# Kernel tuning notes

Hardware: AMD Instinct MI355X
Metric: run time of the kernel (lower is better)

## Reference

```python
import jax, jax.numpy as jnp
import numpy as np

NUM_HEADS = 16


def setup_inputs() -> dict:
    key = jax.random.key(0)
    k1, k2, k3 = jax.random.split(key, 3)
    S, B, E = 2048, 4, 1024
    std = float(np.sqrt(2.0 / (E + E)))
    query = jax.random.normal(k1, (S, B, E), dtype=jnp.float32)
    in_proj_weight = jax.random.normal(k2, (3 * E, E), dtype=jnp.float32) * std
    in_proj_bias = jnp.zeros((3 * E,), dtype=jnp.float32)
    out_proj_weight = jax.random.normal(k3, (E, E), dtype=jnp.float32) * std
    out_proj_bias = jnp.zeros((E,), dtype=jnp.float32)
    return {
        "query": query,
        "in_proj_weight": in_proj_weight,
        "in_proj_bias": in_proj_bias,
        "out_proj_weight": out_proj_weight,
        "out_proj_bias": out_proj_bias,
    }


def reference(query, in_proj_weight, in_proj_bias, out_proj_weight, out_proj_bias):
    S, B, E = query.shape
    H = NUM_HEADS
    hd = E // H
    scale = hd ** -0.5
    # fused QKV projection: [S, B, 3E]
    lin = jnp.einsum("sbe,fe->sbf", query, in_proj_weight) + in_proj_bias
    # torch layout: view(S, B*H, 3, hd) -> interleaved [h, {q,k,v}, hd]
    lin = lin.reshape(S, B * H, 3, hd)
    q = lin[:, :, 0, :]  # [S, B*H, hd]
    k = lin[:, :, 1, :]
    v = lin[:, :, 2, :]
    # scores: [B*H, S_q, S_k]
    scores = jnp.einsum("sbd,tbd->bst", q, k) * scale
    attn = jax.nn.softmax(scores.astype(jnp.float32), axis=-1).astype(scores.dtype)
    # context: [S, B*H, hd] -> [S, B, E]
    ctx = jnp.einsum("bst,tbd->sbd", attn, v).reshape(S, B, E)
    out = jnp.einsum("sbe,fe->sbf", ctx, out_proj_weight) + out_proj_bias
    return out
```

## Files before the change

### kernel.cpp

```cpp
#include <hip/hip_runtime.h>
#include <hip/hip_bf16.h>

typedef __hip_bfloat16 bf16;
typedef __attribute__((ext_vector_type(8))) short short8;
typedef __attribute__((ext_vector_type(4))) float floatx4;

#define GLD_LDS(g, l) __builtin_amdgcn_global_load_lds( \
    (const __attribute__((address_space(1))) void*)(g), \
    (__attribute__((address_space(3))) void*)(l), 16, 0, 0)

#define CS 0.18033688f

__global__ __launch_bounds__(256)
void cvt3_kernel(const float* __restrict__ q,  bf16* __restrict__ qo,
                 const float* __restrict__ w1, bf16* __restrict__ w1o,
                 const float* __restrict__ w2, bf16* __restrict__ w2o)
{
    const int i = blockIdx.x * 256 + threadIdx.x;
    const float* src; bf16* dst; long off;
    if (i < 1048576)       { src = q;  dst = qo;  off = (long)i * 8; }
    else if (i < 1441792)  { src = w1; dst = w1o; off = (long)(i - 1048576) * 8; }
    else                   { src = w2; dst = w2o; off = (long)(i - 1441792) * 8; }
    floatx4 a = *(const floatx4*)(src + off);
    floatx4 b = *(const floatx4*)(src + off + 4);
    short8 h;
    #pragma unroll
    for (int e = 0; e < 4; ++e) {
        union { bf16 v; short s; } u0, u1;
        u0.v = __float2bfloat16(a[e]); h[e]     = u0.s;
        u1.v = __float2bfloat16(b[e]); h[e + 4] = u1.s;
    }
    *(short8*)(dst + off) = h;
}

__device__ __forceinline__ void stage_f32(const float* __restrict__ src, int ld,
                                          bf16* lds, int t)
{
    const int sr = t >> 1;
    const int sc = (t & 1) * 16;
    const float* g = src + (long)sr * ld + sc;
    floatx4 f[4];
    #pragma unroll
    for (int i = 0; i < 4; ++i) f[i] = *(const floatx4*)(g + i * 4);
    short8 h[2];
    #pragma unroll
    for (int v = 0; v < 2; ++v)
        #pragma unroll
        for (int e = 0; e < 8; ++e) {
            union { bf16 b; short s; } u;
            u.b = __float2bfloat16(f[v * 2 + (e >> 2)][e & 3]);
            h[v][e] = u.s;
        }
    *(short8*)(lds + sr * 32 + sc)     = h[0];
    *(short8*)(lds + sr * 32 + sc + 8) = h[1];
}

template<int EPI, int AF32, int BF32>
__global__ __launch_bounds__(256, 2)
void gemm_bt(const void* __restrict__ Ap, const void* __restrict__ Bp,
             const float* __restrict__ bias,
             void* __restrict__ o0, bf16* __restrict__ o1, bf16* __restrict__ o2,
             int K, int N)
{
    __shared__ __align__(16) bf16 lA[128 * 32];
    __shared__ __align__(16) bf16 lB[128 * 32];

    const int t    = threadIdx.x;
    const int lane = t & 63;
    const int w    = t >> 6;
    const int mBase = blockIdx.y * 128;
    const int nBase = blockIdx.x * 128;
    const int wr = (w >> 1) * 64;
    const int wc = (w & 1) * 64;

    const int rowL = t >> 2;
    const int colL = (t & 3) * 8;
    const bf16* gA0 = (const bf16*)Ap + (long)(mBase + rowL) * K + colL;
    const bf16* gA1 = (const bf16*)Ap + (long)(mBase + rowL + 64) * K + colL;
    const bf16* gB0 = (const bf16*)Bp + (long)(nBase + rowL) * K + colL;
    const bf16* gB1 = (const bf16*)Bp + (long)(nBase + rowL + 64) * K + colL;
    char* lAb = (char*)lA + w * 1024;
    char* lBb = (char*)lB + w * 1024;

    floatx4 acc[4][4] = {};

    for (int k0 = 0; k0 < K; k0 += 32) {
        if constexpr (AF32) {
            stage_f32((const float*)Ap + (long)mBase * K + k0, K, lA, t);
        } else {
            GLD_LDS(gA0 + k0, lAb);
            GLD_LDS(gA1 + k0, lAb + 4096);
        }
        if constexpr (BF32) {
            stage_f32((const float*)Bp + (long)nBase * K + k0, K, lB, t);
        } else {
            GLD_LDS(gB0 + k0, lBb);
            GLD_LDS(gB1 + k0, lBb + 4096);
        }
        asm volatile("s_waitcnt vmcnt(0)" ::: "memory");
        __syncthreads();

        short8 af[4], bfr[4];
        #pragma unroll
        for (int m = 0; m < 4; ++m)
            af[m] = *(const short8*)(lA + (wr + m * 16 + (lane & 15)) * 32 + (lane >> 4) * 8);
        #pragma unroll
        for (int n = 0; n < 4; ++n)
            bfr[n] = *(const short8*)(lB + (wc + n * 16 + (lane & 15)) * 32 + (lane >> 4) * 8);
        #pragma unroll
        for (int m = 0; m < 4; ++m)
            #pragma unroll
            for (int n = 0; n < 4; ++n)
                acc[m][n] = __builtin_amdgcn_mfma_f32_16x16x32_bf16(af[m], bfr[n], acc[m][n], 0, 0, 0);
        __syncthreads();
    }

    #pragma unroll
    for (int m = 0; m < 4; ++m) {
        #pragma unroll
        for (int n = 0; n < 4; ++n) {
            const int col = nBase + wc + n * 16 + (lane & 15);
            const int r0  = mBase + wr + m * 16 + ((lane >> 4) << 2);
            const float bv = bias[col];
            if constexpr (EPI == 0) {
                const int h   = col / 192;
                const int rem = col % 192;
                const int qkv = rem >> 6;
                const int d   = rem & 63;
                #pragma unroll
                for (int j = 0; j < 4; ++j) {
                    const int r = r0 + j;
                    const int s = r >> 2;
                    const int b = r & 3;
                    const float v = acc[m][n][j] + bv;
                    if (qkv == 0)
                        ((bf16*)o0)[(((((b << 4) + h) << 11) + s) << 6) + d] =
                            __float2bfloat16(v * CS);
                    else if (qkv == 1)
                        o1[(((((b << 4) + h) << 11) + s) << 6) + d] = __float2bfloat16(v);
                    else
                        o2[((((b << 4) + h) << 17)) + (d << 11) + s] = __float2bfloat16(v);
                }
            } else {
                #pragma unroll
                for (int j = 0; j < 4; ++j)
                    ((float*)o0)[(long)(r0 + j) * N + col] = acc[m][n][j] + bv;
            }
        }
    }
}

__global__ __launch_bounds__(256, 2)
void attn_kernel(const bf16* __restrict__ Q, const bf16* __restrict__ Kg,
                 const bf16* __restrict__ Vt, bf16* __restrict__ Ctx)
{
    __shared__ __align__(16) bf16 lK[2][64 * 64];
    __shared__ __align__(16) bf16 lV[2][64 * 64];

    const int t    = threadIdx.x;
    const int lane = t & 63;
    const int w    = t >> 6;
    const int f    = lane & 15;
    const int g    = lane >> 4;
    const int bh   = blockIdx.y;
    const int q0   = blockIdx.x * 128 + w * 32;
    const long hb  = (long)bh * 2048 * 64;
    const bf16* Qh = Q  + hb;
    const bf16* Kh = Kg + hb;
    const bf16* Vh = Vt + hb;

    const int srow = t >> 3;
    const int scol = (t & 7) * 8;
    const int sig0 = (srow & 3) | ((srow & 16) >> 2) | ((srow & 12) << 1);
    const int wb0 = ((srow)      * 128 + scol * 2) ^ (((srow)      & 7) << 4);
    const int wb1 = ((srow + 32) * 128 + scol * 2) ^ (((srow + 32) & 7) << 4);

    short8 qf[2][2];
    #pragma unroll
    for (int m = 0; m < 2; ++m)
        #pragma unroll
        for (int kk = 0; kk < 2; ++kk)
            qf[m][kk] = *(const short8*)(Qh + (q0 + m * 16 + f) * 64 + kk * 32 + g * 8);

    short8 ones;
    #pragma unroll
    for (int e = 0; e < 8; ++e) ones[e] = (short)0x3F80;

    floatx4 o[2][4] = {};
    floatx4 dn[2] = {};

    short8 kR0 = *(const short8*)(Kh + (long)sig0 * 64 + scol);
    short8 kR1 = *(const short8*)(Kh + (long)(sig0 + 32) * 64 + scol);
    short8 vR0 = *(const short8*)(Vh + (long)srow * 2048 + scol);
    short8 vR1 = *(const short8*)(Vh + (long)(srow + 32) * 2048 + scol);
    *(short8*)((char*)lK[0] + wb0) = kR0;
    *(short8*)((char*)lK[0] + wb1) = kR1;
    *(short8*)((char*)lV[0] + wb0) = vR0;
    *(short8*)((char*)lV[0] + wb1) = vR1;
    kR0 = *(const short8*)(Kh + (long)(64 + sig0) * 64 + scol);
    kR1 = *(const short8*)(Kh + (long)(64 + sig0 + 32) * 64 + scol);
    vR0 = *(const short8*)(Vh + (long)srow * 2048 + 64 + scol);
    vR1 = *(const short8*)(Vh + (long)(srow + 32) * 2048 + 64 + scol);
    __syncthreads();

    auto tile = [&](const bf16* curK, const bf16* curV,
                    bf16* nxtK, bf16* nxtV, int t0) __attribute__((always_inline)) {
        short8 kf[4][2];
        #pragma unroll
        for (int n = 0; n < 4; ++n)
            #pragma unroll
            for (int kk = 0; kk < 2; ++kk) {
                const int key = n * 16 + f;
                const int byte = (key * 128 + kk * 64 + g * 16) ^ ((key & 7) << 4);
                kf[n][kk] = *(const short8*)((const char*)curK + byte);
            }

        if (t0 + 64 < 2048) {
            *(short8*)((char*)nxtK + wb0) = kR0;
            *(short8*)((char*)nxtK + wb1) = kR1;
            *(short8*)((char*)nxtV + wb0) = vR0;
            *(short8*)((char*)nxtV + wb1) = vR1;
        }
        if (t0 + 128 < 2048) {
            kR0 = *(const short8*)(Kh + (long)(t0 + 128 + sig0) * 64 + scol);
            kR1 = *(const short8*)(Kh + (long)(t0 + 128 + sig0 + 32) * 64 + scol);
            vR0 = *(const short8*)(Vh + (long)srow * 2048 + t0 + 128 + scol);
            vR1 = *(const short8*)(Vh + (long)(srow + 32) * 2048 + t0 + 128 + scol);
        }

        floatx4 sa2[4][2] = {};
        __builtin_amdgcn_s_setprio(1);
        #pragma unroll
        for (int n = 0; n < 4; ++n)
            #pragma unroll
            for (int m = 0; m < 2; ++m)
                #pragma unroll
                for (int kk = 0; kk < 2; ++kk)
                    sa2[n][m] = __builtin_amdgcn_mfma_f32_16x16x32_bf16(kf[n][kk], qf[m][kk], sa2[n][m], 0, 0, 0);
        __builtin_amdgcn_s_setprio(0);

        short8 vf[4][2];
        #pragma unroll
        for (int n2 = 0; n2 < 4; ++n2)
            #pragma unroll
            for (int kk = 0; kk < 2; ++kk) {
                const int dim = n2 * 16 + f;
                const int byte = (dim * 128 + kk * 64 + g * 16) ^ ((dim & 7) << 4);
                vf[n2][kk] = *(const short8*)((const char*)curV + byte);
            }

        short8 pf[2][2];
        #pragma unroll
        for (int m = 0; m < 2; ++m)
            #pragma unroll
            for (int kk = 0; kk < 2; ++kk)
                #pragma unroll
                for (int e = 0; e < 8; ++e) {
                    union { bf16 b; short s; } u;
                    u.b = __float2bfloat16(exp2f(sa2[2 * kk + (e >> 2)][m][e & 3]));
                    pf[m][kk][e] = u.s;
                }

        __builtin_amdgcn_s_setprio(1);
        #pragma unroll
        for (int m = 0; m < 2; ++m) {
            #pragma unroll
            for (int n2 = 0; n2 < 4; ++n2)
                #pragma unroll
                for (int kk = 0; kk < 2; ++kk)
                    o[m][n2] = __builtin_amdgcn_mfma_f32_16x16x32_bf16(pf[m][kk], vf[n2][kk], o[m][n2], 0, 0, 0);
            #pragma unroll
            for (int kk = 0; kk < 2; ++kk)
                dn[m] = __builtin_amdgcn_mfma_f32_16x16x32_bf16(pf[m][kk], ones, dn[m], 0, 0, 0);
        }
        __builtin_amdgcn_s_setprio(0);

        __syncthreads();
    };

    for (int t0 = 0; t0 < 2048; t0 += 128) {
        tile(lK[0], lV[0], lK[1], lV[1], t0);
        tile(lK[1], lV[1], lK[0], lV[0], t0 + 64);
    }

    const int b = bh >> 4;
    const int h = bh & 15;
    #pragma unroll
    for (int m = 0; m < 2; ++m) {
        float inv[4];
        #pragma unroll
        for (int j = 0; j < 4; ++j)
            inv[j] = 1.f / dn[m][j];
        #pragma unroll
        for (int n2 = 0; n2 < 4; ++n2) {
            const int dim = (h << 6) + n2 * 16 + f;
            #pragma unroll
            for (int j = 0; j < 4; ++j) {
                const int srw = q0 + m * 16 + (g << 2) + j;
                Ctx[(((srw << 2) + b) << 10) + dim] = __float2bfloat16(o[m][n2][j] * inv[j]);
            }
        }
    }
}

extern "C" void kernel_launch(void* const* d_in, const int* in_sizes, int n_in,
                              void* d_out, int out_size, void* d_ws, size_t ws_size,
                              hipStream_t stream)
{
    const float* query = (const float*)d_in[0];
    const float* wIn   = (const float*)d_in[1];
    const float* bIn   = (const float*)d_in[2];
    const float* wOut  = (const float*)d_in[3];
    const float* bOut  = (const float*)d_in[4];

    const size_t HEADSZ = (size_t)64 * 2048 * 64;
    bf16* Qws = (bf16*)d_ws;
    bf16* Kws = Qws + HEADSZ;
    bf16* Vtw = Kws + HEADSZ;
    bf16* Ctx = Vtw + HEADSZ;
    bf16* qbf = Ctx;
    if (ws_size < 4 * HEADSZ * sizeof(bf16)) return;

    const size_t NEED_BIG = (4 * HEADSZ + 3145728 + 1048576) * sizeof(bf16);
    if (ws_size >= NEED_BIG) {
        bf16* wInBf  = Ctx + HEADSZ;
        bf16* wOutBf = wInBf + 3145728;
        cvt3_kernel<<<dim3(6144), 256, 0, stream>>>(query, qbf, wIn, wInBf, wOut, wOutBf);
        gemm_bt<0, 0, 0><<<dim3(24, 64), 256, 0, stream>>>(qbf, wInBf, bIn,
                                                           Qws, Kws, Vtw, 1024, 3072);
        attn_kernel<<<dim3(16, 64), 256, 0, stream>>>(Qws, Kws, Vtw, Ctx);
        gemm_bt<1, 0, 0><<<dim3(8, 64), 256, 0, stream>>>(Ctx, wOutBf, bOut,
                                                          d_out, nullptr, nullptr, 1024, 1024);
    } else {
        cvt3_kernel<<<dim3(4096), 256, 0, stream>>>(query, qbf, nullptr, nullptr, nullptr, nullptr);
        gemm_bt<0, 0, 1><<<dim3(24, 64), 256, 0, stream>>>(qbf, wIn, bIn,
                                                           Qws, Kws, Vtw, 1024, 3072);
        attn_kernel<<<dim3(16, 64), 256, 0, stream>>>(Qws, Kws, Vtw, Ctx);
        gemm_bt<1, 0, 1><<<dim3(8, 64), 256, 0, stream>>>(Ctx, wOut, bOut,
                                                          d_out, nullptr, nullptr, 1024, 1024);
    }
}
```

Before: 221.1 us.

## Load K/V fragments directly from global memory and remap block order for L2 reuse

Removes the shared-memory staging of K and V tiles and the per-tile block barrier. Each wave now loads its MFMA K fragments straight from global memory, prefetching the next tile into registers, and loads V fragments directly as well. The block index is also remapped so that consecutive blocks cover different heads and query blocks, grouping them for L2 locality. In exchange, each of the four waves redundantly fetches the same K/V data through the cache, and the V loads are no longer prefetched, which can expose their latency.

```diff
diff --git a/kernel.cpp b/kernel.cpp
--- a/kernel.cpp
+++ b/kernel.cpp
@@ -154,27 +154,20 @@
 void attn_kernel(const bf16* __restrict__ Q, const bf16* __restrict__ Kg,
                  const bf16* __restrict__ Vt, bf16* __restrict__ Ctx)
 {
-    __shared__ __align__(16) bf16 lK[2][64 * 64];
-    __shared__ __align__(16) bf16 lV[2][64 * 64];
-
     const int t    = threadIdx.x;
     const int lane = t & 63;
     const int w    = t >> 6;
     const int f    = lane & 15;
     const int g    = lane >> 4;
-    const int bh   = blockIdx.y;
-    const int q0   = blockIdx.x * 128 + w * 32;
+    const int lin  = blockIdx.x + (blockIdx.y << 4);
+    const int qb   = (lin >> 3) & 15;
+    const int bh   = (lin & 7) | ((lin >> 7) << 3);
+    const int q0   = qb * 128 + w * 32;
     const long hb  = (long)bh * 2048 * 64;
     const bf16* Qh = Q  + hb;
     const bf16* Kh = Kg + hb;
     const bf16* Vh = Vt + hb;
 
-    const int srow = t >> 3;
-    const int scol = (t & 7) * 8;
-    const int sig0 = (srow & 3) | ((srow & 16) >> 2) | ((srow & 12) << 1);
-    const int wb0 = ((srow)      * 128 + scol * 2) ^ (((srow)      & 7) << 4);
-    const int wb1 = ((srow + 32) * 128 + scol * 2) ^ (((srow + 32) & 7) << 4);
-
     short8 qf[2][2];
     #pragma unroll
     for (int m = 0; m < 2; ++m)
@@ -182,6 +175,18 @@
         for (int kk = 0; kk < 2; ++kk)
             qf[m][kk] = *(const short8*)(Qh + (q0 + m * 16 + f) * 64 + kk * 32 + g * 8);
 
+    const bf16* kp[4];
+    #pragma unroll
+    for (int n = 0; n < 4; ++n) {
+        const int key = n * 16 + f;
+        const int sk  = (key & 3) | ((key & 16) >> 2) | ((key & 12) << 1) | (key & 32);
+        kp[n] = Kh + (long)sk * 64 + g * 8;
+    }
+    const bf16* vp[4];
+    #pragma unroll
+    for (int n2 = 0; n2 < 4; ++n2)
+        vp[n2] = Vh + (long)(n2 * 16 + f) * 2048 + g * 8;
+
     short8 ones;
     #pragma unroll
     for (int e = 0; e < 8; ++e) ones[e] = (short)0x3F80;
@@ -189,45 +194,15 @@
     floatx4 o[2][4] = {};
     floatx4 dn[2] = {};
 
-    short8 kR0 = *(const short8*)(Kh + (long)sig0 * 64 + scol);
-    short8 kR1 = *(const short8*)(Kh + (long)(sig0 + 32) * 64 + scol);
-    short8 vR0 = *(const short8*)(Vh + (long)srow * 2048 + scol);
-    short8 vR1 = *(const short8*)(Vh + (long)(srow + 32) * 2048 + scol);
-    *(short8*)((char*)lK[0] + wb0) = kR0;
-    *(short8*)((char*)lK[0] + wb1) = kR1;
-    *(short8*)((char*)lV[0] + wb0) = vR0;
-    *(short8*)((char*)lV[0] + wb1) = vR1;
-    kR0 = *(const short8*)(Kh + (long)(64 + sig0) * 64 + scol);
-    kR1 = *(const short8*)(Kh + (long)(64 + sig0 + 32) * 64 + scol);
-    vR0 = *(const short8*)(Vh + (long)srow * 2048 + 64 + scol);
-    vR1 = *(const short8*)(Vh + (long)(srow + 32) * 2048 + 64 + scol);
-    __syncthreads();
-
-    auto tile = [&](const bf16* curK, const bf16* curV,
-                    bf16* nxtK, bf16* nxtV, int t0) __attribute__((always_inline)) {
-        short8 kf[4][2];
-        #pragma unroll
-        for (int n = 0; n < 4; ++n)
-            #pragma unroll
-            for (int kk = 0; kk < 2; ++kk) {
-                const int key = n * 16 + f;
-                const int byte = (key * 128 + kk * 64 + g * 16) ^ ((key & 7) << 4);
-                kf[n][kk] = *(const short8*)((const char*)curK + byte);
-            }
-
-        if (t0 + 64 < 2048) {
-            *(short8*)((char*)nxtK + wb0) = kR0;
-            *(short8*)((char*)nxtK + wb1) = kR1;
-            *(short8*)((char*)nxtV + wb0) = vR0;
-            *(short8*)((char*)nxtV + wb1) = vR1;
-        }
-        if (t0 + 128 < 2048) {
-            kR0 = *(const short8*)(Kh + (long)(t0 + 128 + sig0) * 64 + scol);
-            kR1 = *(const short8*)(Kh + (long)(t0 + 128 + sig0 + 32) * 64 + scol);
-            vR0 = *(const short8*)(Vh + (long)srow * 2048 + t0 + 128 + scol);
-            vR1 = *(const short8*)(Vh + (long)(srow + 32) * 2048 + t0 + 128 + scol);
-        }
-
+    short8 kfA[4][2], kfB[4][2];
+    #pragma unroll
+    for (int n = 0; n < 4; ++n)
+        #pragma unroll
+        for (int kk = 0; kk < 2; ++kk)
+            kfA[n][kk] = *(const short8*)(kp[n] + kk * 32);
+
+    auto tile = [&](short8 (&cur)[4][2], short8 (&nxt)[4][2], int t0)
+        __attribute__((always_inline)) {
         floatx4 sa2[4][2] = {};
         __builtin_amdgcn_s_setprio(1);
         #pragma unroll
@@ -236,18 +211,22 @@
             for (int m = 0; m < 2; ++m)
                 #pragma unroll
                 for (int kk = 0; kk < 2; ++kk)
-                    sa2[n][m] = __builtin_amdgcn_mfma_f32_16x16x32_bf16(kf[n][kk], qf[m][kk], sa2[n][m], 0, 0, 0);
+                    sa2[n][m] = __builtin_amdgcn_mfma_f32_16x16x32_bf16(cur[n][kk], qf[m][kk], sa2[n][m], 0, 0, 0);
         __builtin_amdgcn_s_setprio(0);
 
+        if (t0 + 64 < 2048) {
+            #pragma unroll
+            for (int n = 0; n < 4; ++n)
+                #pragma unroll
+                for (int kk = 0; kk < 2; ++kk)
+                    nxt[n][kk] = *(const short8*)(kp[n] + (long)(t0 + 64) * 64 + kk * 32);
+        }
         short8 vf[4][2];
         #pragma unroll
         for (int n2 = 0; n2 < 4; ++n2)
             #pragma unroll
-            for (int kk = 0; kk < 2; ++kk) {
-                const int dim = n2 * 16 + f;
-                const int byte = (dim * 128 + kk * 64 + g * 16) ^ ((dim & 7) << 4);
-                vf[n2][kk] = *(const short8*)((const char*)curV + byte);
-            }
+            for (int kk = 0; kk < 2; ++kk)
+                vf[n2][kk] = *(const short8*)(vp[n2] + t0 + kk * 32);
 
         short8 pf[2][2];
         #pragma unroll
@@ -274,13 +253,11 @@
                 dn[m] = __builtin_amdgcn_mfma_f32_16x16x32_bf16(pf[m][kk], ones, dn[m], 0, 0, 0);
         }
         __builtin_amdgcn_s_setprio(0);
-
-        __syncthreads();
     };
 
     for (int t0 = 0; t0 < 2048; t0 += 128) {
-        tile(lK[0], lV[0], lK[1], lV[1], t0);
-        tile(lK[1], lV[1], lK[0], lV[0], t0 + 64);
+        tile(kfA, kfB, t0);
+        tile(kfB, kfA, t0 + 64);
     }
 
     const int b = bh >> 4;
```

Result: slower. 348.0 us (+57.4%).

## Load attention K/V tiles directly into LDS with global_load_lds

Applied to the files above, without the earlier changes.

Replaces the register-staged K/V prefetch (global load into registers, then store into swizzled LDS one tile later) with direct global-to-LDS DMA loads. Per-lane source offsets are inverted from the swizzled LDS destination, so each lane fetches the element that belongs at its linear LDS slot. This frees the staging registers and removes the LDS store instructions, at the cost of shortening the prefetch distance from two tiles to one. It also depends on the existing end-of-tile sync to cover the async load completion, which the unseen remainder of the loop may or may not provide.

```diff
diff --git a/kernel.cpp b/kernel.cpp
--- a/kernel.cpp
+++ b/kernel.cpp
@@ -169,11 +169,16 @@
     const bf16* Kh = Kg + hb;
     const bf16* Vh = Vt + hb;
 
-    const int srow = t >> 3;
-    const int scol = (t & 7) * 8;
-    const int sig0 = (srow & 3) | ((srow & 16) >> 2) | ((srow & 12) << 1);
-    const int wb0 = ((srow)      * 128 + scol * 2) ^ (((srow)      & 7) << 4);
-    const int wb1 = ((srow + 32) * 128 + scol * 2) ^ (((srow + 32) & 7) << 4);
+    int koff[2], voff[2];
+    #pragma unroll
+    for (int i = 0; i < 2; ++i) {
+        const int X = t * 16 + i * 4096;
+        const int r = X >> 7;
+        const int c = (X & 127) ^ ((r & 7) << 4);
+        const int sr = (r & 3) | ((r & 16) >> 2) | ((r & 12) << 1) | (r & 32);
+        koff[i] = sr * 64 + (c >> 1);
+        voff[i] = r * 2048 + (c >> 1);
+    }
 
     short8 qf[2][2];
     #pragma unroll
@@ -189,22 +194,24 @@
     floatx4 o[2][4] = {};
     floatx4 dn[2] = {};
 
-    short8 kR0 = *(const short8*)(Kh + (long)sig0 * 64 + scol);
-    short8 kR1 = *(const short8*)(Kh + (long)(sig0 + 32) * 64 + scol);
-    short8 vR0 = *(const short8*)(Vh + (long)srow * 2048 + scol);
-    short8 vR1 = *(const short8*)(Vh + (long)(srow + 32) * 2048 + scol);
-    *(short8*)((char*)lK[0] + wb0) = kR0;
-    *(short8*)((char*)lK[0] + wb1) = kR1;
-    *(short8*)((char*)lV[0] + wb0) = vR0;
-    *(short8*)((char*)lV[0] + wb1) = vR1;
-    kR0 = *(const short8*)(Kh + (long)(64 + sig0) * 64 + scol);
-    kR1 = *(const short8*)(Kh + (long)(64 + sig0 + 32) * 64 + scol);
-    vR0 = *(const short8*)(Vh + (long)srow * 2048 + 64 + scol);
-    vR1 = *(const short8*)(Vh + (long)(srow + 32) * 2048 + 64 + scol);
+    #pragma unroll
+    for (int i = 0; i < 2; ++i) {
+        GLD_LDS(Kh + koff[i], (char*)lK[0] + w * 1024 + i * 4096);
+        GLD_LDS(Vh + voff[i], (char*)lV[0] + w * 1024 + i * 4096);
+    }
+    asm volatile("s_waitcnt vmcnt(0)" ::: "memory");
     __syncthreads();
 
     auto tile = [&](const bf16* curK, const bf16* curV,
                     bf16* nxtK, bf16* nxtV, int t0) __attribute__((always_inline)) {
+        if (t0 + 64 < 2048) {
+            #pragma unroll
+            for (int i = 0; i < 2; ++i) {
+                GLD_LDS(Kh + (long)(t0 + 64) * 64 + koff[i], (char*)nxtK + w * 1024 + i * 4096);
+                GLD_LDS(Vh + voff[i] + (t0 + 64),            (char*)nxtV + w * 1024 + i * 4096);
+            }
+        }
+
         short8 kf[4][2];
         #pragma unroll
         for (int n = 0; n < 4; ++n)
@@ -214,19 +221,6 @@
                 const int byte = (key * 128 + kk * 64 + g * 16) ^ ((key & 7) << 4);
                 kf[n][kk] = *(const short8*)((const char*)curK + byte);
             }
-
-        if (t0 + 64 < 2048) {
-            *(short8*)((char*)nxtK + wb0) = kR0;
-            *(short8*)((char*)nxtK + wb1) = kR1;
-            *(short8*)((char*)nxtV + wb0) = vR0;
-            *(short8*)((char*)nxtV + wb1) = vR1;
-        }
-        if (t0 + 128 < 2048) {
-            kR0 = *(const short8*)(Kh + (long)(t0 + 128 + sig0) * 64 + scol);
-            kR1 = *(const short8*)(Kh + (long)(t0 + 128 + sig0 + 32) * 64 + scol);
-            vR0 = *(const short8*)(Vh + (long)srow * 2048 + t0 + 128 + scol);
-            vR1 = *(const short8*)(Vh + (long)(srow + 32) * 2048 + t0 + 128 + scol);
-        }
 
         floatx4 sa2[4][2] = {};
         __builtin_amdgcn_s_setprio(1);
```

Result: no change. 225.2 us (+1.9%).
